# Performance work log

Measured on AMD Instinct MI355X. Metric: run time of the kernel, lower is better.

Reference implementation:

```python
import jax, jax.numpy as jnp
import numpy as np

N = 12288      # number of nodes
D = 256        # in_features
K = 31         # k_neighbours + 1
EPS = 1e-12    # F.normalize eps


def setup_inputs() -> dict:
    key = jax.random.key(0)
    k1, k2, k3 = jax.random.split(key, 3)
    x = jax.random.normal(k1, (N, D), dtype=jnp.float32)
    # Attentive layer params: elementwise feature weights (torch init is ones;
    # perturb so the reference is non-degenerate)
    w0 = 1.0 + 0.1 * jax.random.normal(k2, (D,), dtype=jnp.float32)
    w1 = 1.0 + 0.1 * jax.random.normal(k3, (D,), dtype=jnp.float32)
    return {"x": x, "w0": w0, "w1": w1}


def reference(x, w0, w1):
    # internal_forward: relu(Attentive_0(x)) then Attentive_1 (last layer, no act)
    h = jax.nn.relu(x * w0)          # [N, D]
    h = h * w1                        # [N, D]
    # F.normalize(dim=-1, p=2)
    norm = jnp.sqrt(jnp.sum(h * h, axis=-1, keepdims=True))
    h = h / jnp.maximum(norm, EPS)
    # cal_similarity_graph: dense NxN similarity
    s = jnp.einsum('nd,md->nm', h, h)  # [N, N]
    # graph_top_K: keep top-K entries per row, zero the rest (scatter mask)
    _, idx = jax.lax.top_k(s, K)       # idx: [N, K]
    rows = jnp.arange(s.shape[0])[:, None]
    mask = jnp.zeros_like(s).at[rows, idx].set(1.0)
    # apply_non_linearity 'relu'
    return jax.nn.relu(s * mask)
```

## Files before the change

kernel.cpp:

```cpp
#include <hip/hip_runtime.h>
#include <cstdint>
#include <cstddef>
#include <math.h>

#define N_NODES 12288
#define D_FEAT  256
#define K_TOP   31

__device__ __forceinline__ float np_g(float xv, float w0v, float w1v) {
  #pragma clang fp contract(off)
  float t = __fmul_rn(xv, w0v);
  t = fmaxf(t, 0.0f);
  return __fmul_rn(t, w1v);
}

__global__ __launch_bounds__(256) void np_norm_kernel(
    const float* __restrict__ x, const float* __restrict__ w0,
    const float* __restrict__ w1, float* __restrict__ nrm) {
  #pragma clang fp contract(off)
  const int n = blockIdx.x * blockDim.x + threadIdx.x;
  if (n >= N_NODES) return;
  const float* xr = x + (size_t)n * D_FEAT;
  float blk[2];
  #pragma unroll
  for (int b = 0; b < 2; ++b) {
    float r[8];
    #pragma unroll
    for (int j = 0; j < 8; ++j) {
      const int d = 128 * b + j;
      const float g = np_g(xr[d], w0[d], w1[d]);
      r[j] = __fmul_rn(g, g);
    }
    for (int i = 8; i < 128; i += 8) {
      #pragma unroll
      for (int j = 0; j < 8; ++j) {
        const int d = 128 * b + i + j;
        const float g = np_g(xr[d], w0[d], w1[d]);
        r[j] = __fadd_rn(r[j], __fmul_rn(g, g));
      }
    }
    blk[b] = __fadd_rn(
        __fadd_rn(__fadd_rn(r[0], r[1]), __fadd_rn(r[2], r[3])),
        __fadd_rn(__fadd_rn(r[4], r[5]), __fadd_rn(r[6], r[7])));
  }
  const float tot = __fadd_rn(blk[0], blk[1]);
  nrm[n] = fmaxf(__fsqrt_rn(tot), 1e-12f);
}

#define BT 128
#define BK 32
#define TBW 132
#define NTILES (N_NODES / BT)
#define NBLOCKS (NTILES * (NTILES + 1) / 2)

__global__ __launch_bounds__(256, 4) void np_gemm_kernel(
    const float* __restrict__ x, const float* __restrict__ w0,
    const float* __restrict__ w1, const float* __restrict__ nrm,
    float* __restrict__ out) {
  #pragma clang fp contract(off)
  __shared__ __align__(16) float smem[64 * TBW];
  float (*As)[BT] = reinterpret_cast<float (*)[BT]>(smem);
  float (*Bs)[BT] = reinterpret_cast<float (*)[BT]>(smem + BK * BT);
  float (*tb)[TBW] = reinterpret_cast<float (*)[TBW]>(smem);

  const int L = blockIdx.x;
  int by = (int)(96.5 - sqrt(96.5 * 96.5 - 2.0 * (double)L));
  while (by > 0 && by * NTILES - by * (by - 1) / 2 > L) --by;
  while ((by + 1) * NTILES - (by + 1) * by / 2 <= L) ++by;
  const int bx = by + (L - (by * NTILES - by * (by - 1) / 2));

  const int n0 = by * BT;
  const int m0 = bx * BT;
  const int t = threadIdx.x;
  const int tx = t & 15, ty = t >> 4;
  const int sr = t >> 1;
  const int sk = (t & 1) * 16;

  float acc[8][8] = {};

  for (int k0 = 0; k0 < D_FEAT; k0 += BK) {
    __syncthreads();
    {
      const float ia = nrm[n0 + sr];
      const float ib = nrm[m0 + sr];
      #pragma unroll
      for (int q = 0; q < 4; ++q) {
        const int c = sk + q * 4;
        const float4 xa = *reinterpret_cast<const float4*>(
            &x[(size_t)(n0 + sr) * D_FEAT + k0 + c]);
        const float4 xb = *reinterpret_cast<const float4*>(
            &x[(size_t)(m0 + sr) * D_FEAT + k0 + c]);
        const float4 wa = *reinterpret_cast<const float4*>(&w0[k0 + c]);
        const float4 wb = *reinterpret_cast<const float4*>(&w1[k0 + c]);
        const float xaf[4] = {xa.x, xa.y, xa.z, xa.w};
        const float xbf[4] = {xb.x, xb.y, xb.z, xb.w};
        const float w0f[4] = {wa.x, wa.y, wa.z, wa.w};
        const float w1f[4] = {wb.x, wb.y, wb.z, wb.w};
        #pragma unroll
        for (int e = 0; e < 4; ++e) {
          As[c + e][sr] = __fdiv_rn(np_g(xaf[e], w0f[e], w1f[e]), ia);
          Bs[c + e][sr] = __fdiv_rn(np_g(xbf[e], w0f[e], w1f[e]), ib);
        }
      }
    }
    __syncthreads();

    for (int kk = 0; kk < BK; ++kk) {
      const float4 a0 = *reinterpret_cast<const float4*>(&As[kk][ty * 4]);
      const float4 a1 = *reinterpret_cast<const float4*>(&As[kk][64 + ty * 4]);
      const float4 b0 = *reinterpret_cast<const float4*>(&Bs[kk][tx * 4]);
      const float4 b1 = *reinterpret_cast<const float4*>(&Bs[kk][64 + tx * 4]);
      const float af[8] = {a0.x, a0.y, a0.z, a0.w, a1.x, a1.y, a1.z, a1.w};
      const float bf[8] = {b0.x, b0.y, b0.z, b0.w, b1.x, b1.y, b1.z, b1.w};
      #pragma unroll
      for (int i = 0; i < 8; ++i)
        #pragma unroll
        for (int j = 0; j < 8; ++j)
          acc[i][j] = __builtin_fmaf(af[i], bf[j], acc[i][j]);
    }
  }

  #pragma unroll
  for (int i = 0; i < 8; ++i) {
    const int row = n0 + (i >> 2) * 64 + ty * 4 + (i & 3);
    float4 o0, o1;
    o0.x = acc[i][0]; o0.y = acc[i][1]; o0.z = acc[i][2]; o0.w = acc[i][3];
    o1.x = acc[i][4]; o1.y = acc[i][5]; o1.z = acc[i][6]; o1.w = acc[i][7];
    *reinterpret_cast<float4*>(&out[(size_t)row * N_NODES + m0 + tx * 4]) = o0;
    *reinterpret_cast<float4*>(&out[(size_t)row * N_NODES + m0 + 64 + tx * 4]) = o1;
  }

  if (bx != by) {
    #pragma unroll
    for (int hh = 0; hh < 2; ++hh) {
      __syncthreads();
      #pragma unroll
      for (int r = 0; r < 4; ++r) {
        const int j = hh * 4 + r;
        const int ml = tx * 4 + r;
        #pragma unroll
        for (int ih = 0; ih < 2; ++ih) {
          float4 v;
          v.x = acc[ih * 4 + 0][j];
          v.y = acc[ih * 4 + 1][j];
          v.z = acc[ih * 4 + 2][j];
          v.w = acc[ih * 4 + 3][j];
          *reinterpret_cast<float4*>(&tb[ml][ih * 64 + ty * 4]) = v;
        }
      }
      __syncthreads();
      #pragma unroll
      for (int p = 0; p < 8; ++p) {
        const int row = (t >> 5) + 8 * p;
        const int col = (t & 31) * 4;
        const float4 v = *reinterpret_cast<const float4*>(&tb[row][col]);
        *reinterpret_cast<float4*>(
            &out[(size_t)(m0 + hh * 64 + row) * N_NODES + n0 + col]) = v;
      }
    }
  }
}

__device__ inline float att_decode(unsigned uu) {
  return (uu & 0x80000000u) ? __uint_as_float(uu & 0x7FFFFFFFu)
                            : __uint_as_float(~uu);
}

#define HBINS 2048

__global__ __launch_bounds__(256) void att_topk_kernel(float* __restrict__ s) {
  const int n = blockIdx.x;
  float* row = s + (size_t)n * N_NODES;
  const int t = threadIdx.x;
  const int lane = t & 63, wid = t >> 6;

  unsigned u[48];
#pragma unroll
  for (int i = 0; i < 12; ++i) {
    float4 v = reinterpret_cast<const float4*>(row)[t + 256 * i];
    const float f[4] = {v.x, v.y, v.z, v.w};
#pragma unroll
    for (int j = 0; j < 4; ++j) {
      unsigned b = __float_as_uint(f[j]);
      u[i * 4 + j] = (b & 0x80000000u) ? ~b : (b | 0x80000000u);
    }
  }

  __shared__ unsigned hist[HBINS];
  __shared__ unsigned wmn[4], wmx[4];
  __shared__ int wred[4];
  __shared__ unsigned bc_mn, bc_mx, bc_T;
  __shared__ int bc_B, bc_above, bc_cnt, bc_cand;
  __shared__ int cnt_s;

  unsigned mymn = u[0], mymx = u[0];
#pragma unroll
  for (int i = 1; i < 48; ++i) {
    mymn = u[i] < mymn ? u[i] : mymn;
    mymx = u[i] > mymx ? u[i] : mymx;
  }
#pragma unroll
  for (int o = 32; o > 0; o >>= 1) {
    const unsigned a = __shfl_down(mymn, o);
    const unsigned b = __shfl_down(mymx, o);
    mymn = a < mymn ? a : mymn;
    mymx = b > mymx ? b : mymx;
  }
  if (lane == 0) { wmn[wid] = mymn; wmx[wid] = mymx; }
  __syncthreads();
  if (t == 0) {
    unsigned mn = wmn[0], mx = wmx[0];
    for (int w = 1; w < 4; ++w) {
      mn = wmn[w] < mn ? wmn[w] : mn;
      mx = wmx[w] > mx ? wmx[w] : mx;
    }
    bc_mn = mn; bc_mx = mx;
  }
  __syncthreads();

  unsigned T;
  if (bc_mn == bc_mx) {
    T = bc_mn;
  } else {
    unsigned cur_lo = bc_mn;
    unsigned cur_range = bc_mx - bc_mn;
    int above_total = 0;
    bool done = false;
    for (int pass = 0; pass < 4 && !done; ++pass) {
      const int bits = 32 - __clz(cur_range);
      const int sh = bits > 11 ? bits - 11 : 0;
#pragma unroll
      for (int q = 0; q < HBINS / 256; ++q) hist[t + 256 * q] = 0u;
      __syncthreads();
#pragma unroll
      for (int i = 0; i < 48; ++i) {
        const unsigned rel = u[i] - cur_lo;
        if (u[i] >= cur_lo && rel <= cur_range)
          atomicAdd(&hist[rel >> sh], 1u);
      }
      __syncthreads();
      int hloc[8];
      int part = 0;
#pragma unroll
      for (int q = 0; q < 8; ++q) { hloc[q] = (int)hist[8 * t + q]; part += hloc[q]; }
      int v = part;
#pragma unroll
      for (int o = 1; o < 64; o <<= 1) {
        const int z = __shfl_down(v, o);
        if (lane + o < 64) v += z;
      }
      if (lane == 0) wred[wid] = v;
      __syncthreads();
      int wsuf = 0;
      for (int w = wid + 1; w < 4; ++w) wsuf += wred[w];
      const int suffix_incl = v + wsuf;
      int run = suffix_incl - part;
      int fB = -1, fAbove = 0, fCnt = 0;
#pragma unroll
      for (int q = 7; q >= 0; --q) {
        const int above = run;
        const int cnt = hloc[q];
        if (cnt > 0 && above_total + above < K_TOP &&
            above_total + above + cnt >= K_TOP) {
          fB = 8 * t + q; fAbove = above; fCnt = cnt;
        }
        run += cnt;
      }
      if (fB >= 0) { bc_B = fB; bc_above = fAbove; bc_cnt = fCnt; }
      __syncthreads();
      const int B = bc_B;
      const int aboveB = bc_above;
      const int cntB = bc_cnt;
      const unsigned bin_lo = cur_lo + ((unsigned)B << sh);
      if (sh == 0) {
        T = bin_lo;
        done = true;
      } else if (cntB <= HBINS) {
        if (t == 0) bc_cand = 0;
        __syncthreads();
#pragma unroll
        for (int i = 0; i < 48; ++i) {
          const unsigned rel = u[i] - cur_lo;
          if (u[i] >= cur_lo && rel <= cur_range && (int)(rel >> sh) == B) {
            const int slot = atomicAdd(&bc_cand, 1);
            hist[slot] = u[i];
          }
        }
        __syncthreads();
        const int m = bc_cand;
        const int kb = K_TOP - above_total - aboveB;
        for (int e = t; e < m; e += 256) {
          const unsigned ce = hist[e];
          int gt = 0, eq = 0;
          for (int e2 = 0; e2 < m; ++e2) {
            const unsigned c2 = hist[e2];
            gt += (c2 > ce) ? 1 : 0;
            eq += (c2 == ce) ? 1 : 0;
          }
          if (gt < kb && gt + eq >= kb) bc_T = ce;
        }
        __syncthreads();
        T = bc_T;
        done = true;
      } else {
        above_total += aboveB;
        cur_lo = bin_lo;
        cur_range = (1u << sh) - 1u;
      }
      __syncthreads();
    }
  }

  {
    int cg = 0, ce = 0;
#pragma unroll
    for (int i = 0; i < 48; ++i) {
      cg += (u[i] > T) ? 1 : 0;
      ce += (u[i] == T) ? 1 : 0;
    }
    int packed = (cg << 16) | ce;
#pragma unroll
    for (int o = 32; o > 0; o >>= 1) packed += __shfl_down(packed, o);
    if (t == 0) cnt_s = 0;
    __syncthreads();
    if ((t & 63) == 0) atomicAdd(&cnt_s, packed);
    __syncthreads();
  }
  const int tot = cnt_s;
  __syncthreads();
  const int tot_gt = tot >> 16;
  const int tot_eq = tot & 0xFFFF;
  const int need = K_TOP - tot_gt;

  if (tot_eq == need) {
#pragma unroll
    for (int i = 0; i < 12; ++i) {
      float vals[4];
#pragma unroll
      for (int j = 0; j < 4; ++j) {
        const unsigned uu = u[i * 4 + j];
        const float f = att_decode(uu);
        vals[j] = (uu >= T) ? fmaxf(f, 0.0f) : 0.0f;
      }
      float4 o; o.x = vals[0]; o.y = vals[1]; o.z = vals[2]; o.w = vals[3];
      reinterpret_cast<float4*>(row)[t + 256 * i] = o;
    }
  } else {
    __shared__ int eqc[12][256];
#pragma unroll
    for (int i = 0; i < 12; ++i) {
      int c = 0;
#pragma unroll
      for (int j = 0; j < 4; ++j) c += (u[i * 4 + j] == T) ? 1 : 0;
      eqc[i][t] = c;
    }
    __syncthreads();
    int base[12];
    {
      int run = 0;
      for (int i = 0; i < 12; ++i) {
        int pre = 0, tt_tot = 0;
        for (int tt = 0; tt < 256; ++tt) {
          const int vv = eqc[i][tt];
          if (tt < t) pre += vv;
          tt_tot += vv;
        }
        base[i] = run + pre;
        run += tt_tot;
      }
    }
#pragma unroll
    for (int i = 0; i < 12; ++i) {
      float vals[4];
      int r = base[i];
#pragma unroll
      for (int j = 0; j < 4; ++j) {
        const unsigned uu = u[i * 4 + j];
        const float f = att_decode(uu);
        bool keep = false;
        if (uu > T) keep = true;
        else if (uu == T) { keep = (r < need); ++r; }
        vals[j] = keep ? fmaxf(f, 0.0f) : 0.0f;
      }
      float4 o; o.x = vals[0]; o.y = vals[1]; o.z = vals[2]; o.w = vals[3];
      reinterpret_cast<float4*>(row)[t + 256 * i] = o;
    }
  }
}

extern "C" void kernel_launch(void* const* d_in, const int* in_sizes, int n_in,
                              void* d_out, int out_size, void* d_ws, size_t ws_size,
                              hipStream_t stream) {
  const float* x  = (const float*)d_in[0];
  const float* w0 = (const float*)d_in[1];
  const float* w1 = (const float*)d_in[2];
  float* out = (float*)d_out;
  float* nrm = (float*)d_ws;

  np_norm_kernel<<<N_NODES / 256, 256, 0, stream>>>(x, w0, w1, nrm);

  np_gemm_kernel<<<NBLOCKS, 256, 0, stream>>>(x, w0, w1, nrm, out);

  att_topk_kernel<<<N_NODES, 256, 0, stream>>>(out);
}
```

Measured before the change: 870.8 us.

## Precompute normalized features once and use nontemporal stores for similarity output

Adds a kernel that writes the normalized, weighted features h to workspace once, so the GEMM tiles load h directly instead of recomputing relu, scale and division per tile. The GEMM output stores become nontemporal, and the launch-bounds occupancy hint drops from 4 to 2. The precompute path runs only when the workspace is large enough; otherwise it falls back to the old fused path. The trade is an extra pass over an N×D buffer, plus a risk that nontemporal stores evict the output from cache before the top-k kernel reads it back.

```diff
diff --git a/kernel.cpp b/kernel.cpp
--- a/kernel.cpp
+++ b/kernel.cpp
@@ -6,12 +6,20 @@
 #define N_NODES 12288
 #define D_FEAT  256
 #define K_TOP   31
+
+typedef float nfloat4 __attribute__((ext_vector_type(4)));
 
 __device__ __forceinline__ float np_g(float xv, float w0v, float w1v) {
   #pragma clang fp contract(off)
   float t = __fmul_rn(xv, w0v);
   t = fmaxf(t, 0.0f);
   return __fmul_rn(t, w1v);
+}
+
+__device__ __forceinline__ void nt_store4(float* p, float4 v) {
+  nfloat4 nv;
+  nv.x = v.x; nv.y = v.y; nv.z = v.z; nv.w = v.w;
+  __builtin_nontemporal_store(nv, reinterpret_cast<nfloat4*>(p));
 }
 
 __global__ __launch_bounds__(256) void np_norm_kernel(
@@ -47,16 +55,39 @@
   nrm[n] = fmaxf(__fsqrt_rn(tot), 1e-12f);
 }
 
+__global__ __launch_bounds__(256) void np_h_kernel(
+    const float* __restrict__ x, const float* __restrict__ w0,
+    const float* __restrict__ w1, const float* __restrict__ nrm,
+    float* __restrict__ h) {
+  #pragma clang fp contract(off)
+  const int q = blockIdx.x * blockDim.x + threadIdx.x;
+  const int base = q * 4;
+  if (base >= N_NODES * D_FEAT) return;
+  const int n = base >> 8;
+  const int d = base & (D_FEAT - 1);
+  const float ia = nrm[n];
+  const float4 xv = *reinterpret_cast<const float4*>(&x[base]);
+  const float4 w0v = *reinterpret_cast<const float4*>(&w0[d]);
+  const float4 w1v = *reinterpret_cast<const float4*>(&w1[d]);
+  float4 o;
+  o.x = __fdiv_rn(np_g(xv.x, w0v.x, w1v.x), ia);
+  o.y = __fdiv_rn(np_g(xv.y, w0v.y, w1v.y), ia);
+  o.z = __fdiv_rn(np_g(xv.z, w0v.z, w1v.z), ia);
+  o.w = __fdiv_rn(np_g(xv.w, w0v.w, w1v.w), ia);
+  *reinterpret_cast<float4*>(&h[base]) = o;
+}
+
 #define BT 128
 #define BK 32
 #define TBW 132
 #define NTILES (N_NODES / BT)
 #define NBLOCKS (NTILES * (NTILES + 1) / 2)
 
-__global__ __launch_bounds__(256, 4) void np_gemm_kernel(
+template <int PRE>
+__global__ __launch_bounds__(256, 2) void np_gemm_kernel(
     const float* __restrict__ x, const float* __restrict__ w0,
     const float* __restrict__ w1, const float* __restrict__ nrm,
-    float* __restrict__ out) {
+    const float* __restrict__ h, float* __restrict__ out) {
   #pragma clang fp contract(off)
   __shared__ __align__(16) float smem[64 * TBW];
   float (*As)[BT] = reinterpret_cast<float (*)[BT]>(smem);
@@ -80,7 +111,20 @@
 
   for (int k0 = 0; k0 < D_FEAT; k0 += BK) {
     __syncthreads();
-    {
+    if (PRE) {
+      #pragma unroll
+      for (int q = 0; q < 4; ++q) {
+        const int c = sk + q * 4;
+        const float4 ha = *reinterpret_cast<const float4*>(
+            &h[(size_t)(n0 + sr) * D_FEAT + k0 + c]);
+        const float4 hb = *reinterpret_cast<const float4*>(
+            &h[(size_t)(m0 + sr) * D_FEAT + k0 + c]);
+        As[c + 0][sr] = ha.x; As[c + 1][sr] = ha.y;
+        As[c + 2][sr] = ha.z; As[c + 3][sr] = ha.w;
+        Bs[c + 0][sr] = hb.x; Bs[c + 1][sr] = hb.y;
+        Bs[c + 2][sr] = hb.z; Bs[c + 3][sr] = hb.w;
+      }
+    } else {
       const float ia = nrm[n0 + sr];
       const float ib = nrm[m0 + sr];
       #pragma unroll
@@ -126,8 +170,8 @@
     float4 o0, o1;
     o0.x = acc[i][0]; o0.y = acc[i][1]; o0.z = acc[i][2]; o0.w = acc[i][3];
     o1.x = acc[i][4]; o1.y = acc[i][5]; o1.z = acc[i][6]; o1.w = acc[i][7];
-    *reinterpret_cast<float4*>(&out[(size_t)row * N_NODES + m0 + tx * 4]) = o0;
-    *reinterpret_cast<float4*>(&out[(size_t)row * N_NODES + m0 + 64 + tx * 4]) = o1;
+    nt_store4(&out[(size_t)row * N_NODES + m0 + tx * 4], o0);
+    nt_store4(&out[(size_t)row * N_NODES + m0 + 64 + tx * 4], o1);
   }
 
   if (bx != by) {
@@ -154,8 +198,7 @@
         const int row = (t >> 5) + 8 * p;
         const int col = (t & 31) * 4;
         const float4 v = *reinterpret_cast<const float4*>(&tb[row][col]);
-        *reinterpret_cast<float4*>(
-            &out[(size_t)(m0 + hh * 64 + row) * N_NODES + n0 + col]) = v;
+        nt_store4(&out[(size_t)(m0 + hh * 64 + row) * N_NODES + n0 + col], v);
       }
     }
   }
@@ -396,10 +439,19 @@
   const float* w1 = (const float*)d_in[2];
   float* out = (float*)d_out;
   float* nrm = (float*)d_ws;
+  float* h = (float*)((char*)d_ws + 65536);
+
+  const size_t need = 65536 + (size_t)N_NODES * D_FEAT * 4;
 
   np_norm_kernel<<<N_NODES / 256, 256, 0, stream>>>(x, w0, w1, nrm);
 
-  np_gemm_kernel<<<NBLOCKS, 256, 0, stream>>>(x, w0, w1, nrm, out);
+  if (ws_size >= need) {
+    np_h_kernel<<<(N_NODES * D_FEAT / 4 + 255) / 256, 256, 0, stream>>>(
+        x, w0, w1, nrm, h);
+    np_gemm_kernel<1><<<NBLOCKS, 256, 0, stream>>>(x, w0, w1, nrm, h, out);
+  } else {
+    np_gemm_kernel<0><<<NBLOCKS, 256, 0, stream>>>(x, w0, w1, nrm, nullptr, out);
+  }
 
   att_topk_kernel<<<N_NODES, 256, 0, stream>>>(out);
 }
```

Measured after the change: 701.6 us. -19.4%, faster.
